# Kernel tuning notes

Measured on AMD Instinct MI355X. Metric: run time of the kernel, lower is better.

The kernel has to match this reference:

```python
import jax, jax.numpy as jnp
import numpy as np

D_MODEL = 1024
N_HEADS = 16
D_HEAD = D_MODEL // N_HEADS


def setup_inputs() -> dict:
    key = jax.random.key(0)
    ks = jax.random.split(key, 11)
    B, S = 2, 2048
    s_in = 1.0 / np.sqrt(D_MODEL)
    return {
        "query": jax.random.normal(ks[0], (B, S, D_MODEL), jnp.float32),
        "key": jax.random.normal(ks[1], (B, S, D_MODEL), jnp.float32),
        "value": jax.random.normal(ks[2], (B, S, D_MODEL), jnp.float32),
        "Wq_w": jax.random.normal(ks[3], (D_MODEL, D_MODEL), jnp.float32) * s_in,
        "Wq_b": jax.random.normal(ks[4], (D_MODEL,), jnp.float32) * 0.01,
        "Wk_w": jax.random.normal(ks[5], (D_HEAD, D_MODEL), jnp.float32) * s_in,
        "Wk_b": jax.random.normal(ks[6], (D_HEAD,), jnp.float32) * 0.01,
        "Wv_w": jax.random.normal(ks[7], (D_HEAD, D_MODEL), jnp.float32) * s_in,
        "Wv_b": jax.random.normal(ks[8], (D_HEAD,), jnp.float32) * 0.01,
        "Wo_w": jax.random.normal(ks[9], (D_MODEL, D_MODEL), jnp.float32) * s_in,
        "Wo_b": jax.random.normal(ks[10], (D_MODEL,), jnp.float32) * 0.01,
    }


def reference(query, key, value, Wq_w, Wq_b, Wk_w, Wk_b, Wv_w, Wv_b, Wo_w, Wo_b):
    B, S, _ = query.shape
    # Q: per-head projection [B, H, S, dh]; K/V: single shared head [B, S, dh]
    Q = (query @ Wq_w.T + Wq_b).reshape(B, S, N_HEADS, D_HEAD).transpose(0, 2, 1, 3)
    K = key @ Wk_w.T + Wk_b      # [B, S, dh], shared across heads (MQA)
    V = value @ Wv_w.T + Wv_b    # [B, S, dh]
    scale = 1.0 / np.sqrt(D_HEAD).astype(np.float32)
    scores = jnp.einsum('bhqd,bkd->bhqk', Q, K) * scale  # [B, H, S, S]
    attn = jax.nn.softmax(scores, axis=-1)
    ctx = jnp.einsum('bhqk,bkd->bhqd', attn, V)           # [B, H, S, dh]
    ctx = ctx.transpose(0, 2, 1, 3).reshape(B, S, D_MODEL)
    out = ctx @ Wo_w.T + Wo_b
    return out, attn
```

## Files before the change

kernel.cpp:

```cpp
#include <hip/hip_runtime.h>
#include <hip/hip_bf16.h>
#include <math.h>

#define D_MODEL 1024
#define N_HEADS 16
#define D_HEAD 64
#define S_ 2048

typedef __attribute__((ext_vector_type(8))) short short8;
typedef __attribute__((ext_vector_type(4))) float f32x4;
typedef __attribute__((ext_vector_type(16))) float f32x16;

static __device__ inline short f2bf(float f) {
    union { __hip_bfloat16 h; short s; } u;
    u.h = __float2bfloat16(f);
    return u.s;
}

static __device__ inline unsigned pk_bf16(float a, float b) {
    unsigned r;
    asm("v_cvt_pk_bf16_f32 %0, %1, %2" : "=v"(r) : "v"(a), "v"(b));
    return r;
}

static __device__ inline f32x4 mfma16(short8 a, short8 b, f32x4 c) {
    return __builtin_amdgcn_mfma_f32_16x16x32_bf16(a, b, c, 0, 0, 0);
}
static __device__ inline f32x16 mfma32(short8 a, short8 b, f32x16 c) {
    return __builtin_amdgcn_mfma_f32_32x32x16_bf16(a, b, c, 0, 0, 0);
}
static __device__ inline f32x16 zero16() {
    f32x16 z;
#pragma unroll
    for (int i = 0; i < 16; i++) z[i] = 0.f;
    return z;
}

static __device__ inline void load_lds16(const void* g, void* l) {
    __builtin_amdgcn_global_load_lds(
        (const __attribute__((address_space(1))) unsigned int*)g,
        (__attribute__((address_space(3))) unsigned int*)l, 16, 0, 0);
}

__global__ __launch_bounds__(256)
void cvt_all(const float* __restrict__ q, const float* __restrict__ k,
             const float* __restrict__ v, const float* __restrict__ wq,
             const float* __restrict__ wk, const float* __restrict__ wv,
             const float* __restrict__ wo,
             short* dq, short* dk, short* dv, short* dwq, short* dwk,
             short* dwv, short* dwo) {
    size_t c = (size_t)blockIdx.x * 256 + threadIdx.x;
    const float* s; short* d; size_t off;
    if (c < 524288)        { s = q;  d = dq;  off = c; }
    else if (c < 1048576)  { s = k;  d = dk;  off = c - 524288; }
    else if (c < 1572864)  { s = v;  d = dv;  off = c - 1048576; }
    else if (c < 1703936)  { s = wq; d = dwq; off = c - 1572864; }
    else if (c < 1712128)  { s = wk; d = dwk; off = c - 1703936; }
    else if (c < 1720320)  { s = wv; d = dwv; off = c - 1712128; }
    else                   { s = wo; d = dwo; off = c - 1720320; }
    const f32x4* sp = (const f32x4*)(s + off * 8);
    f32x4 a = sp[0], b = sp[1];
    short8 o;
    o[0] = f2bf(a[0]); o[1] = f2bf(a[1]); o[2] = f2bf(a[2]); o[3] = f2bf(a[3]);
    o[4] = f2bf(b[0]); o[5] = f2bf(b[1]); o[6] = f2bf(b[2]); o[7] = f2bf(b[3]);
    *(short8*)(d + off * 8) = o;
}

template<int BM, int BN, int OUT_MODE>
__device__ __forceinline__ void gemm_body(
    const short* __restrict__ A, const short* __restrict__ Wb,
    const float* __restrict__ bias, void* __restrict__ Cv,
    int bx, int by, int M, int N, int K, float out_scale, char* lds)
{
    constexpr int NI = BM / 32, NJ = BN / 32;
    constexpr int AISS = BM / 32, WISS = BN / 32;
    char* As = lds;
    char* Ws = lds + 2 * BM * 128;
    const int t = threadIdx.x, lane = t & 63, w = t >> 6;
    const int wr = w >> 1, wc = w & 1, r15 = lane & 15, g = lane >> 4;
    const int m0 = by * BM, n0 = bx * BN;
    const size_t Kb2 = (size_t)K * 2;

    int aR[AISS > WISS ? AISS : WISS], aC[AISS > WISS ? AISS : WISS];
#pragma unroll
    for (int i = 0; i < (AISS > WISS ? AISS : WISS); i++) {
        int l = i * 4096 + t * 16;
        aR[i] = l >> 7;
        aC[i] = (l & 127) ^ (((l >> 7) & 7) << 4);
    }

    f32x4 acc[NI][NJ];
#pragma unroll
    for (int i = 0; i < NI; i++)
#pragma unroll
        for (int j = 0; j < NJ; j++) acc[i][j] = (f32x4){0.f, 0.f, 0.f, 0.f};

    const int nk = K / 64;
    auto stage = [&](int kt, int buf) {
        size_t kb = (size_t)kt * 128;
#pragma unroll
        for (int i = 0; i < AISS; i++)
            load_lds16((const char*)A + (size_t)(m0 + aR[i]) * Kb2 + kb + aC[i],
                       As + buf * (BM * 128) + i * 4096 + (w << 10));
#pragma unroll
        for (int i = 0; i < WISS; i++)
            load_lds16((const char*)Wb + (size_t)(n0 + aR[i]) * Kb2 + kb + aC[i],
                       Ws + buf * (BN * 128) + i * 4096 + (w << 10));
    };

    stage(0, 0);
    __syncthreads();
    int cur = 0;
    for (int kt = 0; kt < nk; kt++) {
        if (kt + 1 < nk) stage(kt + 1, cur ^ 1);
        const char* Ab = As + cur * (BM * 128);
        const char* Wbs = Ws + cur * (BN * 128);
#pragma unroll
        for (int kc = 0; kc < 2; kc++) {
            short8 af[NI], bw[NJ];
#pragma unroll
            for (int i = 0; i < NI; i++) {
                int r = wr * (16 * NI) + i * 16 + r15;
                af[i] = *(const short8*)(Ab + r * 128 + ((kc * 64 + g * 16) ^ ((r & 7) << 4)));
            }
#pragma unroll
            for (int j = 0; j < NJ; j++) {
                int r = wc * (16 * NJ) + j * 16 + r15;
                bw[j] = *(const short8*)(Wbs + r * 128 + ((kc * 64 + g * 16) ^ ((r & 7) << 4)));
            }
#pragma unroll
            for (int i = 0; i < NI; i++)
#pragma unroll
                for (int j = 0; j < NJ; j++)
                    acc[i][j] = mfma16(af[i], bw[j], acc[i][j]);
        }
        __syncthreads();
        cur ^= 1;
    }

#pragma unroll
    for (int i = 0; i < NI; i++) {
#pragma unroll
        for (int j = 0; j < NJ; j++) {
            int ncol = n0 + wc * (16 * NJ) + j * 16 + r15;
            float bv = bias[ncol];
#pragma unroll
            for (int reg = 0; reg < 4; reg++) {
                int mrow = m0 + wr * (16 * NI) + i * 16 + g * 4 + reg;
                float val = (acc[i][j][reg] + bv) * out_scale;
                if (OUT_MODE == 0) {
                    __builtin_nontemporal_store(val, (float*)Cv + (size_t)mrow * N + ncol);
                } else if (OUT_MODE == 1) {
                    ((short*)Cv)[(size_t)mrow * N + ncol] = f2bf(val);
                } else {
                    int sb = mrow & 2047;
                    int scol = (sb & ~63) | ((sb & 31) << 1) | ((sb & 32) >> 5);
                    ((short*)Cv)[((((size_t)(mrow >> 11)) * 64 + ncol) << 11) + scol] =
                        f2bf(val);
                }
            }
        }
    }
}

__global__ __launch_bounds__(256)
void qkv_proj(const short* __restrict__ qin, const short* __restrict__ kin,
              const short* __restrict__ vin, const short* __restrict__ wqb,
              const short* __restrict__ wkb, const short* __restrict__ wvb,
              const float* __restrict__ bq, const float* __restrict__ bk,
              const float* __restrict__ bv,
              short* Qb, short* Kb, short* Vtb) {
    __shared__ char lds[49152];
    int bid = blockIdx.x;
    if (bid < 512)
        gemm_body<64, 128, 1>(qin, wqb, bq, Qb, bid & 7, bid >> 3,
                              4096, 1024, 1024, 0.18033688011112f, lds);
    else if (bid < 576)
        gemm_body<64, 64, 1>(kin, wkb, bk, Kb, 0, bid - 512,
                             4096, 64, 1024, 1.0f, lds);
    else
        gemm_body<64, 64, 2>(vin, wvb, bv, Vtb, 0, bid - 576,
                             4096, 64, 1024, 1.0f, lds);
}

__global__ __launch_bounds__(256)
void o_proj(const short* __restrict__ ctxb, const short* __restrict__ wob,
            const float* __restrict__ bo, float* __restrict__ out) {
    __shared__ char lds[49152];
    gemm_body<64, 128, 0>(ctxb, wob, bo, out, blockIdx.x & 7, blockIdx.x >> 3,
                          4096, 1024, 1024, 1.0f, lds);
}

__global__ __launch_bounds__(128)
void mqa_attn6(const short* __restrict__ Qb,
               const short* __restrict__ Kb,
               const short* __restrict__ Vtb,
               float* __restrict__ attn,
               short* __restrict__ ctxb)
{
    __shared__ short KB2[2][4096];
    __shared__ short VB2[2][4096];
    __shared__ short Ps[4096];

    const int t = threadIdx.x, lane = t & 63, w = t >> 6;
    const int l31 = lane & 31, h5 = lane >> 5;
    const int bid = blockIdx.x;
    const int qt = bid & 31, h = (bid >> 5) & 15, b = bid >> 9;
    const int q0 = qt * 64;
    const int wq = w * 32;

    short8 aq[4];
    {
        const char* qbase = (const char*)(Qb +
            (size_t)(b * S_ + q0 + wq + l31) * D_MODEL + h * 64);
#pragma unroll
        for (int kc = 0; kc < 4; kc++)
            aq[kc] = *(const short8*)(qbase + kc * 32 + h5 * 16);
    }

    int koA[4];
    const char* vrowp[4];
#pragma unroll
    for (int i = 0; i < 4; i++) {
        int l = i * 2048 + t * 16;
        int row = l >> 7;
        koA[i] = l ^ ((row & 7) << 4);
        int vc = (l & 127) ^ ((row & 7) << 4);
        vrowp[i] = (const char*)(Vtb + (((size_t)(b * 64 + row)) << 11)) + vc;
    }
    const char* ktile0 = (const char*)(Kb + (size_t)b * S_ * 64);

#define STAGE_K(kti, buf) {                                                    \
        const char* kb_ = ktile0 + (size_t)(kti) * 8192;                       \
        load_lds16(kb_ + koA[0], (char*)KB2 + (buf) * 8192 + 0 * 2048 + (w << 10)); \
        load_lds16(kb_ + koA[1], (char*)KB2 + (buf) * 8192 + 1 * 2048 + (w << 10)); \
        load_lds16(kb_ + koA[2], (char*)KB2 + (buf) * 8192 + 2 * 2048 + (w << 10)); \
        load_lds16(kb_ + koA[3], (char*)KB2 + (buf) * 8192 + 3 * 2048 + (w << 10)); }
#define STAGE_V(kti, buf) {                                                    \
        load_lds16(vrowp[0] + (size_t)(kti) * 128, (char*)VB2 + (buf) * 8192 + 0 * 2048 + (w << 10)); \
        load_lds16(vrowp[1] + (size_t)(kti) * 128, (char*)VB2 + (buf) * 8192 + 1 * 2048 + (w << 10)); \
        load_lds16(vrowp[2] + (size_t)(kti) * 128, (char*)VB2 + (buf) * 8192 + 2 * 2048 + (w << 10)); \
        load_lds16(vrowp[3] + (size_t)(kti) * 128, (char*)VB2 + (buf) * 8192 + 3 * 2048 + (w << 10)); }
#define RD(base, r, cb) (*(const short8*)((const char*)(base) + (r) * 128 + ((cb) ^ (((r) & 7) << 4))))

    float lsum[16];
#pragma unroll
    for (int reg = 0; reg < 16; reg++) lsum[reg] = 0.f;

    int cur = 0;
    STAGE_K(0, 0);
    __syncthreads();
    for (int kti = 0; kti < 32; kti++) {
        if (kti + 1 < 32) STAGE_K(kti + 1, cur ^ 1);
        f32x16 s0 = zero16(), s1 = zero16();
        __builtin_amdgcn_s_setprio(1);
#pragma unroll
        for (int kc = 0; kc < 4; kc++) {
            s0 = mfma32(aq[kc], RD(KB2[cur], l31, kc * 32 + h5 * 16), s0);
            s1 = mfma32(aq[kc], RD(KB2[cur], 32 + l31, kc * 32 + h5 * 16), s1);
        }
        __builtin_amdgcn_s_setprio(0);
#pragma unroll
        for (int reg = 0; reg < 16; reg++)
            lsum[reg] += exp2f(s0[reg]) + exp2f(s1[reg]);
        __syncthreads();
        cur ^= 1;
    }

    float c_[16];
#pragma unroll
    for (int reg = 0; reg < 16; reg++) {
        float v = lsum[reg];
        v += __shfl_xor(v, 1); v += __shfl_xor(v, 2);
        v += __shfl_xor(v, 4); v += __shfl_xor(v, 8); v += __shfl_xor(v, 16);
        c_[reg] = -log2f(v);
    }

    f32x16 ctxA = zero16(), ctxB = zero16();
    float* attn_base = attn +
        (((size_t)((b * 16 + h) * 2048 + q0 + wq + 4 * h5)) << 11) + l31;

    cur = 0;
    STAGE_K(0, 0);
    STAGE_V(0, 0);
    __syncthreads();
    for (int kti = 0; kti < 32; kti++) {
        if (kti + 1 < 32) { STAGE_K(kti + 1, cur ^ 1); STAGE_V(kti + 1, cur ^ 1); }
        f32x16 s0, s1;
#pragma unroll
        for (int reg = 0; reg < 16; reg++) { s0[reg] = c_[reg]; s1[reg] = c_[reg]; }
        __builtin_amdgcn_s_setprio(1);
#pragma unroll
        for (int kc = 0; kc < 4; kc++) {
            s0 = mfma32(aq[kc], RD(KB2[cur], l31, kc * 32 + h5 * 16), s0);
            s1 = mfma32(aq[kc], RD(KB2[cur], 32 + l31, kc * 32 + h5 * 16), s1);
        }
        __builtin_amdgcn_s_setprio(0);
        float* arowptr = attn_base + (size_t)kti * 64;
#pragma unroll
        for (int reg = 0; reg < 16; reg++) {
            const int rloc = (reg & 3) + 8 * (reg >> 2);
            const int rps = wq + rloc + 4 * h5;
            float p0 = exp2f(s0[reg]);
            float p1 = exp2f(s1[reg]);
            __builtin_nontemporal_store(p0, arowptr + ((size_t)rloc << 11));
            __builtin_nontemporal_store(p1, arowptr + ((size_t)rloc << 11) + 32);
            *(unsigned*)((char*)Ps + rps * 128 + ((4 * l31) ^ ((rps & 7) << 4))) =
                pk_bf16(p0, p1);
        }
        short8 ap[4];
#pragma unroll
        for (int kc = 0; kc < 4; kc++)
            ap[kc] = RD(Ps, wq + l31, kc * 32 + h5 * 16);
        __builtin_amdgcn_s_setprio(1);
#pragma unroll
        for (int kc = 0; kc < 4; kc++) {
            ctxA = mfma32(ap[kc], RD(VB2[cur], l31, kc * 32 + h5 * 16), ctxA);
            ctxB = mfma32(ap[kc], RD(VB2[cur], 32 + l31, kc * 32 + h5 * 16), ctxB);
        }
        __builtin_amdgcn_s_setprio(0);
        __syncthreads();
        cur ^= 1;
    }

    const int tokbase = b * 2048 + q0 + wq + 4 * h5;
#pragma unroll
    for (int reg = 0; reg < 16; reg++) {
        const int rloc = (reg & 3) + 8 * (reg >> 2);
        size_t base = (size_t)(tokbase + rloc) * D_MODEL + h * 64 + l31;
        ctxb[base]      = f2bf(ctxA[reg]);
        ctxb[base + 32] = f2bf(ctxB[reg]);
    }
#undef STAGE_K
#undef STAGE_V
#undef RD
}

extern "C" void kernel_launch(void* const* d_in, const int* in_sizes, int n_in,
                              void* d_out, int out_size, void* d_ws, size_t ws_size,
                              hipStream_t stream) {
    const float* query = (const float*)d_in[0];
    const float* key   = (const float*)d_in[1];
    const float* value = (const float*)d_in[2];
    const float* Wq_w  = (const float*)d_in[3];
    const float* Wq_b  = (const float*)d_in[4];
    const float* Wk_w  = (const float*)d_in[5];
    const float* Wk_b  = (const float*)d_in[6];
    const float* Wv_w  = (const float*)d_in[7];
    const float* Wv_b  = (const float*)d_in[8];
    const float* Wo_w  = (const float*)d_in[9];
    const float* Wo_b  = (const float*)d_in[10];

    short* ws   = (short*)d_ws;
    short* qin  = ws;
    short* kin  = qin  + (size_t)4194304;
    short* vin  = kin  + (size_t)4194304;
    short* wqb  = vin  + (size_t)4194304;
    short* wkb  = wqb  + (size_t)1048576;
    short* wvb  = wkb  + (size_t)65536;
    short* wob  = wvb  + (size_t)65536;
    short* Qb   = wob  + (size_t)1048576;
    short* Kb   = Qb   + (size_t)4194304;
    short* Vtb  = Kb   + (size_t)262144;
    short* ctxb = Vtb  + (size_t)262144;

    float* out  = (float*)d_out;
    float* attn = out + (size_t)4096 * 1024;

    dim3 blk(256);

    cvt_all<<<dim3(7232), blk, 0, stream>>>(query, key, value, Wq_w, Wk_w, Wv_w,
                                            Wo_w, qin, kin, vin, wqb, wkb, wvb, wob);
    qkv_proj<<<dim3(640), blk, 0, stream>>>(qin, kin, vin, wqb, wkb, wvb,
                                            Wq_b, Wk_b, Wv_b, Qb, Kb, Vtb);
    mqa_attn6<<<dim3(1024), dim3(128), 0, stream>>>(Qb, Kb, Vtb, attn, ctxb);
    o_proj<<<dim3(512), blk, 0, stream>>>(ctxb, wob, Wo_b, out);
}
```

Measured before the change: 221.5 us.

## Split softmax row-sum pass into separate kernel before attention output kernel

Moves the first pass, which computes the per-row sum of exponentials and its negative log, out of the attention kernel into its own kernel that writes results to a workspace buffer. The main attention kernel then loads these normalizers and performs only the probability-write and PV pass. This lowers register and LDS pressure in each kernel, which may raise occupancy and reduce the serialisation of the two passes. The cost is an extra launch and a second read of Q and K.

Result: slower. 240.5 us (+8.6%).

```diff
diff --git a/kernel.cpp b/kernel.cpp
--- a/kernel.cpp
+++ b/kernel.cpp
@@ -192,9 +192,86 @@
 }
 
 __global__ __launch_bounds__(128)
-void mqa_attn6(const short* __restrict__ Qb,
+void mqa_sumexp(const short* __restrict__ Qb,
+                const short* __restrict__ Kb,
+                float* __restrict__ nls)
+{
+    __shared__ short KB2[2][4096];
+
+    const int t = threadIdx.x, lane = t & 63, w = t >> 6;
+    const int l31 = lane & 31, h5 = lane >> 5;
+    const int bid = blockIdx.x;
+    const int qt = bid & 31, h = (bid >> 5) & 15, b = bid >> 9;
+    const int q0 = qt * 64;
+    const int wq = w * 32;
+
+    short8 aq[4];
+    {
+        const char* qbase = (const char*)(Qb +
+            (size_t)(b * S_ + q0 + wq + l31) * D_MODEL + h * 64);
+#pragma unroll
+        for (int kc = 0; kc < 4; kc++)
+            aq[kc] = *(const short8*)(qbase + kc * 32 + h5 * 16);
+    }
+
+    int koA[4];
+#pragma unroll
+    for (int i = 0; i < 4; i++) {
+        int l = i * 2048 + t * 16;
+        koA[i] = l ^ (((l >> 7) & 7) << 4);
+    }
+    const char* ktile0 = (const char*)(Kb + (size_t)b * S_ * 64);
+
+#define STAGE_K(kti, buf) {                                                    \
+        const char* kb_ = ktile0 + (size_t)(kti) * 8192;                       \
+        load_lds16(kb_ + koA[0], (char*)KB2 + (buf) * 8192 + 0 * 2048 + (w << 10)); \
+        load_lds16(kb_ + koA[1], (char*)KB2 + (buf) * 8192 + 1 * 2048 + (w << 10)); \
+        load_lds16(kb_ + koA[2], (char*)KB2 + (buf) * 8192 + 2 * 2048 + (w << 10)); \
+        load_lds16(kb_ + koA[3], (char*)KB2 + (buf) * 8192 + 3 * 2048 + (w << 10)); }
+#define RD(base, r, cb) (*(const short8*)((const char*)(base) + (r) * 128 + ((cb) ^ (((r) & 7) << 4))))
+
+    float lsum[16];
+#pragma unroll
+    for (int reg = 0; reg < 16; reg++) lsum[reg] = 0.f;
+
+    int cur = 0;
+    STAGE_K(0, 0);
+    __syncthreads();
+    for (int kti = 0; kti < 32; kti++) {
+        if (kti + 1 < 32) STAGE_K(kti + 1, cur ^ 1);
+        f32x16 s0 = zero16(), s1 = zero16();
+        __builtin_amdgcn_s_setprio(1);
+#pragma unroll
+        for (int kc = 0; kc < 4; kc++) {
+            s0 = mfma32(aq[kc], RD(KB2[cur], l31, kc * 32 + h5 * 16), s0);
+            s1 = mfma32(aq[kc], RD(KB2[cur], 32 + l31, kc * 32 + h5 * 16), s1);
+        }
+        __builtin_amdgcn_s_setprio(0);
+#pragma unroll
+        for (int reg = 0; reg < 16; reg++)
+            lsum[reg] += exp2f(s0[reg]) + exp2f(s1[reg]);
+        __syncthreads();
+        cur ^= 1;
+    }
+
+    float* nlb = nls + ((size_t)(b * 16 + h) << 11) + q0 + wq + 4 * h5;
+#pragma unroll
+    for (int reg = 0; reg < 16; reg++) {
+        float v = lsum[reg];
+        v += __shfl_xor(v, 1); v += __shfl_xor(v, 2);
+        v += __shfl_xor(v, 4); v += __shfl_xor(v, 8); v += __shfl_xor(v, 16);
+        if (l31 == 0)
+            nlb[(reg & 3) + 8 * (reg >> 2)] = -log2f(v);
+    }
+#undef STAGE_K
+#undef RD
+}
+
+__global__ __launch_bounds__(128)
+void mqa_attn8(const short* __restrict__ Qb,
                const short* __restrict__ Kb,
                const short* __restrict__ Vtb,
+               const float* __restrict__ nls,
                float* __restrict__ attn,
                short* __restrict__ ctxb)
 {
@@ -216,6 +293,14 @@
 #pragma unroll
         for (int kc = 0; kc < 4; kc++)
             aq[kc] = *(const short8*)(qbase + kc * 32 + h5 * 16);
+    }
+
+    float c_[16];
+    {
+        const float* nlb = nls + ((size_t)(b * 16 + h) << 11) + q0 + wq + 4 * h5;
+#pragma unroll
+        for (int reg = 0; reg < 16; reg++)
+            c_[reg] = nlb[(reg & 3) + 8 * (reg >> 2)];
     }
 
     int koA[4];
@@ -243,44 +328,11 @@
         load_lds16(vrowp[3] + (size_t)(kti) * 128, (char*)VB2 + (buf) * 8192 + 3 * 2048 + (w << 10)); }
 #define RD(base, r, cb) (*(const short8*)((const char*)(base) + (r) * 128 + ((cb) ^ (((r) & 7) << 4))))
 
-    float lsum[16];
-#pragma unroll
-    for (int reg = 0; reg < 16; reg++) lsum[reg] = 0.f;
-
-    int cur = 0;
-    STAGE_K(0, 0);
-    __syncthreads();
-    for (int kti = 0; kti < 32; kti++) {
-        if (kti + 1 < 32) STAGE_K(kti + 1, cur ^ 1);
-        f32x16 s0 = zero16(), s1 = zero16();
-        __builtin_amdgcn_s_setprio(1);
-#pragma unroll
-        for (int kc = 0; kc < 4; kc++) {
-            s0 = mfma32(aq[kc], RD(KB2[cur], l31, kc * 32 + h5 * 16), s0);
-            s1 = mfma32(aq[kc], RD(KB2[cur], 32 + l31, kc * 32 + h5 * 16), s1);
-        }
-        __builtin_amdgcn_s_setprio(0);
-#pragma unroll
-        for (int reg = 0; reg < 16; reg++)
-            lsum[reg] += exp2f(s0[reg]) + exp2f(s1[reg]);
-        __syncthreads();
-        cur ^= 1;
-    }
-
-    float c_[16];
-#pragma unroll
-    for (int reg = 0; reg < 16; reg++) {
-        float v = lsum[reg];
-        v += __shfl_xor(v, 1); v += __shfl_xor(v, 2);
-        v += __shfl_xor(v, 4); v += __shfl_xor(v, 8); v += __shfl_xor(v, 16);
-        c_[reg] = -log2f(v);
-    }
-
     f32x16 ctxA = zero16(), ctxB = zero16();
     float* attn_base = attn +
         (((size_t)((b * 16 + h) * 2048 + q0 + wq + 4 * h5)) << 11) + l31;
 
-    cur = 0;
+    int cur = 0;
     STAGE_K(0, 0);
     STAGE_V(0, 0);
     __syncthreads();
@@ -363,6 +415,7 @@
     short* Kb   = Qb   + (size_t)4194304;
     short* Vtb  = Kb   + (size_t)262144;
     short* ctxb = Vtb  + (size_t)262144;
+    float* nls  = (float*)(ctxb + (size_t)4194304);
 
     float* out  = (float*)d_out;
     float* attn = out + (size_t)4096 * 1024;
@@ -373,6 +426,7 @@
                                             Wo_w, qin, kin, vin, wqb, wkb, wvb, wob);
     qkv_proj<<<dim3(640), blk, 0, stream>>>(qin, kin, vin, wqb, wkb, wvb,
                                             Wq_b, Wk_b, Wv_b, Qb, Kb, Vtb);
-    mqa_attn6<<<dim3(1024), dim3(128), 0, stream>>>(Qb, Kb, Vtb, attn, ctxb);
+    mqa_sumexp<<<dim3(1024), dim3(128), 0, stream>>>(Qb, Kb, nls);
+    mqa_attn8<<<dim3(1024), dim3(128), 0, stream>>>(Qb, Kb, Vtb, nls, attn, ctxb);
     o_proj<<<dim3(512), blk, 0, stream>>>(ctxb, wob, Wo_b, out);
 }
```
